# Kernel tuning notes

Hardware: AMD Instinct MI355X
Metric: run time of the kernel (lower is better)

## Reference

```python
import jax, jax.numpy as jnp
import numpy as np

N, n, D1, D2 = 16, 1024, 64, 64


def setup_inputs() -> dict:
    key = jax.random.key(0)
    ks = jax.random.split(key, 17)
    f = lambda k, shape: jax.random.normal(k, shape, dtype=jnp.float32)
    return {
        "A": f(ks[0], (N, n, n)),
        "X": f(ks[1], (N, n, D1)),
        "coeffs": f(ks[2], (5,)),
        "wA1": f(ks[3], (1, D1)),
        "wA2": f(ks[4], (1, D1)),
        "w11": f(ks[5], (D2, D1)),
        "w12": f(ks[6], (D2, D1)),
        "w13": f(ks[7], (D2, 1)),
        "w14": f(ks[8], (D2, 1)),
        "w15": f(ks[9], (D2, 1)),
        "w16": f(ks[10], (D2, 1)),
        "w21": f(ks[11], (D2, D1)),
        "w22": f(ks[12], (D2, D1)),
        "w23": f(ks[13], (D2, 1)),
        "w24": f(ks[14], (D2, 1)),
        "w25": f(ks[15], (D2, 1)),
        "w26": f(ks[16], (D2, 1)),
    }


def reference(A, X, coeffs, wA1, wA2, w11, w12, w13, w14, w15, w16,
              w21, w22, w23, w24, w25, w26):
    nn_ = A.shape[-1]
    diag = jnp.diagonal(A, axis1=-2, axis2=-1)          # (N, n)
    mean_diag = diag.mean(-1)                            # (N,)
    rowmean = A.mean(-1)                                 # (N, n) mean over columns
    mean_all = rowmean.mean(-1)                          # (N,)
    mean_X = X.mean(1)                                   # (N, D1)

    p1 = X @ wA1[0]                                      # (N, n)   Linear(D1->1) per node
    p2 = mean_X @ wA2[0]                                 # (N,)     Linear(D1->1) on mean

    # adjacency transform: scalar-weighted A + scalar stats + symmetrized row stats
    A_t = (coeffs[0] * A
           + (coeffs[1] * mean_all + coeffs[2] * mean_diag + p2)[:, None, None]
           + coeffs[3] * (rowmean[:, None, :] + rowmean[:, :, None])
           + coeffs[4] * (diag[:, None, :] + diag[:, :, None])
           + p1[:, None, :] + p1[:, :, None])             # (N, n, n)

    def node_transform(w_x, w_mx, w_col, w_diag, w_mdiag, w_mall):
        per_graph = (mean_X @ w_mx.T                      # (N, D2)
                     + mean_diag[:, None] * w_mdiag[:, 0][None, :]
                     + mean_all[:, None] * w_mall[:, 0][None, :])
        return (jnp.einsum('bnd,ed->bne', X, w_x)         # (N, n, D2)
                + rowmean[:, :, None] * w_col[:, 0]
                + diag[:, :, None] * w_diag[:, 0]
                + per_graph[:, None, :])

    X1_t = node_transform(w11, w12, w13, w14, w15, w16)
    X2_t = node_transform(w21, w22, w23, w24, w25, w26)

    out = A_t @ X2_t / nn_ + X1_t                         # (N, n, D2)
    return (A_t, out)
```

## Files before the change

kernel.cpp:

```cpp
#include <hip/hip_runtime.h>
#include <hip/hip_bf16.h>

#define NGRAPH 16
#define NNODE 1024
#define DDIM 64

typedef __attribute__((ext_vector_type(8))) short bf16x8;
typedef __attribute__((ext_vector_type(4))) float f32x4;

#define OFF_ROWSUM 0
#define OFF_DIAG   16384
#define OFF_P1     32768
#define OFF_R      49152
#define OFF_CS     65536
#define OFF_S      73728
#define OFF_PG1    73792
#define OFF_PG2    74816
#define OFF_S2P    75840
#define OFF_R2P    92224
#define OFF_S2N    108608
#define OFF_R2N    109632
#define OFF_BASE0  110656
#define OFF_X2T    1159232

__device__ __forceinline__ unsigned short f2bf(float f) {
    unsigned int u = __float_as_uint(f);
    u = (u + 0x7fffu + ((u >> 16) & 1u)) >> 16;
    return (unsigned short)u;
}

__device__ __forceinline__ float wave_reduce(float v) {
    #pragma unroll
    for (int off = 32; off; off >>= 1) v += __shfl_down(v, off, 64);
    return v;
}

__global__ __launch_bounds__(256) void k1_rowstats(const float* __restrict__ A,
                                                   float* __restrict__ rowsum,
                                                   float* __restrict__ diagv) {
    int row  = blockIdx.x * 4 + (threadIdx.x >> 6);
    int lane = threadIdx.x & 63;
    const float4* b4 = (const float4*)(A + (size_t)row * NNODE);
    float sum = 0.f;
    #pragma unroll
    for (int it = 0; it < 4; ++it) {
        float4 v = b4[lane + it * 64];
        sum += v.x + v.y + v.z + v.w;
    }
    sum = wave_reduce(sum);
    if (lane == 0) {
        rowsum[row] = sum;
        int i = row & (NNODE - 1);
        diagv[row] = ((const float*)b4)[i];
    }
}

__global__ __launch_bounds__(256) void k1b_xstats(const float* __restrict__ X,
                                                  const float* __restrict__ wA1,
                                                  float* __restrict__ p1,
                                                  float* __restrict__ colsum_part) {
    int b    = blockIdx.x >> 3;
    int blk  = blockIdx.x & 7;
    int wv   = threadIdx.x >> 6;
    int lane = threadIdx.x & 63;
    float w = wA1[lane];
    float cs = 0.f;
    int row0 = blk * 128 + wv * 32;
    const float* Xb = X + (size_t)b * NNODE * DDIM;
    for (int rI = 0; rI < 32; ++rI) {
        int i = row0 + rI;
        float x = Xb[i * DDIM + lane];
        cs += x;
        float v = wave_reduce(x * w);
        if (lane == 0) p1[b * NNODE + i] = v;
    }
    __shared__ float csl[4][64];
    csl[wv][lane] = cs;
    __syncthreads();
    if (threadIdx.x < 64) {
        float t = csl[0][lane] + csl[1][lane] + csl[2][lane] + csl[3][lane];
        colsum_part[(b * 8 + blk) * 64 + lane] = t;
    }
}

__global__ __launch_bounds__(64) void k2a_graph(const float* __restrict__ rowsum,
                                                const float* __restrict__ diagv,
                                                const float* __restrict__ colsum_part,
                                                const float* __restrict__ coeffs,
                                                const float* __restrict__ wA2,
                                                const float* __restrict__ w12,
                                                const float* __restrict__ w15,
                                                const float* __restrict__ w16,
                                                const float* __restrict__ w22,
                                                const float* __restrict__ w25,
                                                const float* __restrict__ w26,
                                                float* __restrict__ s_out,
                                                float* __restrict__ pg1,
                                                float* __restrict__ pg2) {
    int b = blockIdx.x;
    int lane = threadIdx.x;
    float sa = 0.f, sd = 0.f;
    for (int i = lane; i < NNODE; i += 64) {
        sa += rowsum[b * NNODE + i];
        sd += diagv[b * NNODE + i];
    }
    sa = wave_reduce(sa); sd = wave_reduce(sd);
    sa = __shfl(sa, 0, 64); sd = __shfl(sd, 0, 64);
    float mean_all  = sa * (1.f / ((float)NNODE * (float)NNODE));
    float mean_diag = sd * (1.f / (float)NNODE);

    float mx = 0.f;
    for (int k = 0; k < 8; ++k) mx += colsum_part[(b * 8 + k) * 64 + lane];
    mx *= (1.f / (float)NNODE);
    __shared__ float mxs[64];
    mxs[lane] = mx;
    __syncthreads();

    float p2v = wave_reduce(mx * wA2[lane]);
    p2v = __shfl(p2v, 0, 64);
    float s = coeffs[1] * mean_all + coeffs[2] * mean_diag + p2v;
    if (lane == 0) s_out[b] = s;

    float a1 = 0.f, a2 = 0.f;
    for (int d = 0; d < 64; ++d) {
        float m = mxs[d];
        a1 += m * w12[lane * 64 + d];
        a2 += m * w22[lane * 64 + d];
    }
    pg1[b * 64 + lane] = a1 + mean_diag * w15[lane] + mean_all * w16[lane];
    pg2[b * 64 + lane] = a2 + mean_diag * w25[lane] + mean_all * w26[lane];
}

__global__ __launch_bounds__(256) void k2b_nodes(const float* __restrict__ X,
                                                 const float* __restrict__ coeffs,
                                                 const float* __restrict__ w11,
                                                 const float* __restrict__ w21,
                                                 const float* __restrict__ w13,
                                                 const float* __restrict__ w14,
                                                 const float* __restrict__ w23,
                                                 const float* __restrict__ w24,
                                                 const float* __restrict__ pg1,
                                                 const float* __restrict__ pg2,
                                                 const float* __restrict__ rowsum,
                                                 const float* __restrict__ diagv,
                                                 const float* __restrict__ p1g,
                                                 float* __restrict__ rws,
                                                 float* __restrict__ base0,
                                                 unsigned short* __restrict__ x2tg,
                                                 float* __restrict__ S2part,
                                                 float* __restrict__ R2part) {
    __shared__ float Xl[64][68];
    __shared__ float w1l[64][68];
    __shared__ float w2l[64][68];
    __shared__ unsigned short X2Tl[64][68];
    __shared__ float rm_l[64], dg_l[64], r_l[64];
    __shared__ float redS[4][64], redR[4][64];

    int b    = blockIdx.x >> 4;
    int tile = blockIdx.x & 15;
    int i0   = tile * 64;
    int tid  = threadIdx.x;
    int e    = tid & 63;
    int wv   = tid >> 6;

    const float* Xg = X + (size_t)b * (NNODE * DDIM) + (size_t)i0 * DDIM;
    #pragma unroll
    for (int it = 0; it < 4; ++it) {
        int g   = it * 256 + tid;
        int row = g >> 4;
        int c4  = (g & 15) << 2;
        float4 v  = ((const float4*)Xg)[g];
        *(float4*)&Xl[row][c4] = v;
        float4 v1 = ((const float4*)w11)[g];
        *(float4*)&w1l[row][c4] = v1;
        float4 v2 = ((const float4*)w21)[g];
        *(float4*)&w2l[row][c4] = v2;
    }
    float c3 = coeffs[3], c4c = coeffs[4];
    if (tid < 64) {
        float rs  = rowsum[b * NNODE + i0 + tid];
        float dgv = diagv[b * NNODE + i0 + tid];
        float rmv = rs * (1.f / (float)NNODE);
        rm_l[tid] = rmv;
        dg_l[tid] = dgv;
        float rv = c3 * rmv + c4c * dgv + p1g[b * NNODE + i0 + tid];
        r_l[tid] = rv;
        rws[b * NNODE + i0 + tid] = rv;
    }
    float w13e = w13[e], w14e = w14[e], w23e = w23[e], w24e = w24[e];
    float pg1e = pg1[b * 64 + e], pg2e = pg2[b * 64 + e];
    __syncthreads();

    float acc1[16], acc2[16];
    #pragma unroll
    for (int t = 0; t < 16; ++t) { acc1[t] = 0.f; acc2[t] = 0.f; }

    for (int d0 = 0; d0 < 64; d0 += 4) {
        float4 w1v = *(const float4*)&w1l[e][d0];
        float4 w2v = *(const float4*)&w2l[e][d0];
        #pragma unroll
        for (int t = 0; t < 16; ++t) {
            int li = wv + 4 * t;
            float4 xv = *(const float4*)&Xl[li][d0];
            acc1[t] += xv.x * w1v.x + xv.y * w1v.y + xv.z * w1v.z + xv.w * w1v.w;
            acc2[t] += xv.x * w2v.x + xv.y * w2v.y + xv.z * w2v.z + xv.w * w2v.w;
        }
    }

    float s2acc = 0.f, r2acc = 0.f;
    #pragma unroll
    for (int t = 0; t < 16; ++t) {
        int li = wv + 4 * t;
        int i  = i0 + li;
        float rmv = rm_l[li], dgv = dg_l[li];
        float x2t = acc2[t] + rmv * w23e + dgv * w24e + pg2e;
        float b0  = acc1[t] + rmv * w13e + dgv * w14e + pg1e;
        base0[((size_t)(b * NNODE + i)) * 64 + e] = b0;
        X2Tl[e][li] = f2bf(x2t);
        s2acc += x2t;
        r2acc += r_l[li] * x2t;
    }
    redS[wv][e] = s2acc;
    redR[wv][e] = r2acc;
    __syncthreads();

    for (int k = 0; k < 16; ++k) {
        int ep = wv * 16 + k;
        unsigned short v = X2Tl[ep][e];
        x2tg[((size_t)(b * 64 + ep)) * NNODE + i0 + e] = v;
    }
    if (tid < 64) {
        float s2 = redS[0][tid] + redS[1][tid] + redS[2][tid] + redS[3][tid];
        float r2 = redR[0][tid] + redR[1][tid] + redR[2][tid] + redR[3][tid];
        S2part[(b * 16 + tile) * 64 + tid] = s2;
        R2part[(b * 16 + tile) * 64 + tid] = r2;
    }
}

__global__ __launch_bounds__(64) void k2c_reduce(const float* __restrict__ S2part,
                                                 const float* __restrict__ R2part,
                                                 float* __restrict__ S2n,
                                                 float* __restrict__ R2n) {
    int b = blockIdx.x, e = threadIdx.x;
    float s2 = 0.f, r2 = 0.f;
    for (int t = 0; t < 16; ++t) {
        s2 += S2part[(b * 16 + t) * 64 + e];
        r2 += R2part[(b * 16 + t) * 64 + e];
    }
    S2n[b * 64 + e] = s2 * (1.f / (float)NNODE);
    R2n[b * 64 + e] = r2 * (1.f / (float)NNODE);
}

__global__ __launch_bounds__(256) void k4_main(const float* __restrict__ A,
                                               const float* __restrict__ coeffs,
                                               const float* __restrict__ sArr,
                                               const float* __restrict__ rArr,
                                               const unsigned short* __restrict__ x2tg,
                                               const float* __restrict__ base0,
                                               const float* __restrict__ S2n,
                                               const float* __restrict__ R2n,
                                               float* __restrict__ At,
                                               float* __restrict__ outp) {
    __shared__ unsigned short Al[16][136];
    __shared__ unsigned short X2l[64][136];
    __shared__ float r_lds[1024];

    int b    = blockIdx.x >> 6;
    int tile = blockIdx.x & 63;
    int i0   = tile * 16;
    int tid  = threadIdx.x;

    float4 rv = ((const float4*)(rArr + b * NNODE))[tid];
    *(float4*)&r_lds[tid * 4] = rv;

    float sb  = sArr[b];
    float c0  = coeffs[0];
    float c0n = c0 * (1.f / (float)NNODE);

    int arow = tid >> 4;
    int acol = (tid & 15) * 8;
    const float* Ab  = A  + ((size_t)(b * NNODE + i0 + arow)) * NNODE + acol;
    float*       Atb = At + ((size_t)(b * NNODE + i0 + arow)) * NNODE + acol;
    int xe = tid >> 2;
    int xc = (tid & 3) * 32;
    const unsigned short* X2g = x2tg + ((size_t)(b * 64 + xe)) * NNODE + xc;

    int lane = tid & 63, wv = tid >> 6;
    int m = lane & 15, quad = lane >> 4;
    int e0 = wv << 4;

    f32x4 acc = {0.f, 0.f, 0.f, 0.f};

    for (int kt = 0; kt < 8; ++kt) {
        __syncthreads();

        float4 a0 = *(const float4*)(Ab + kt * 128);
        float4 a1 = *(const float4*)(Ab + kt * 128 + 4);
        float  ri = r_lds[i0 + arow];
        int cidx = kt * 128 + acol;
        float4 rj0 = *(const float4*)&r_lds[cidx];
        float4 rj1 = *(const float4*)&r_lds[cidx + 4];
        float bse = sb + ri;
        float4 t0, t1;
        t0.x = c0 * a0.x + bse + rj0.x; t0.y = c0 * a0.y + bse + rj0.y;
        t0.z = c0 * a0.z + bse + rj0.z; t0.w = c0 * a0.w + bse + rj0.w;
        t1.x = c0 * a1.x + bse + rj1.x; t1.y = c0 * a1.y + bse + rj1.y;
        t1.z = c0 * a1.z + bse + rj1.z; t1.w = c0 * a1.w + bse + rj1.w;
        *(float4*)(Atb + kt * 128)     = t0;
        *(float4*)(Atb + kt * 128 + 4) = t1;

        unsigned int p0 = (unsigned int)f2bf(a0.x) | ((unsigned int)f2bf(a0.y) << 16);
        unsigned int p1 = (unsigned int)f2bf(a0.z) | ((unsigned int)f2bf(a0.w) << 16);
        unsigned int p2 = (unsigned int)f2bf(a1.x) | ((unsigned int)f2bf(a1.y) << 16);
        unsigned int p3 = (unsigned int)f2bf(a1.z) | ((unsigned int)f2bf(a1.w) << 16);
        uint4 pk = {p0, p1, p2, p3};
        *(uint4*)&Al[arow][acol] = pk;

        #pragma unroll
        for (int q = 0; q < 4; ++q) {
            uint4 v = *(const uint4*)(X2g + (size_t)kt * 128 + q * 8);
            *(uint4*)&X2l[xe][xc + q * 8] = v;
        }
        __syncthreads();

        #pragma unroll
        for (int ks = 0; ks < 4; ++ks) {
            int k0 = ks * 32 + quad * 8;
            bf16x8 av = *(const bf16x8*)&Al[m][k0];
            bf16x8 bv = *(const bf16x8*)&X2l[e0 + m][k0];
            acc = __builtin_amdgcn_mfma_f32_16x16x32_bf16(av, bv, acc, 0, 0, 0);
        }
    }

    int e = e0 + m;
    float s2 = S2n[b * 64 + e];
    float r2 = R2n[b * 64 + e];
    #pragma unroll
    for (int reg = 0; reg < 4; ++reg) {
        int i = i0 + quad * 4 + reg;
        float v = acc[reg] * c0n
                + base0[((size_t)(b * NNODE + i)) * 64 + e]
                + (sb + r_lds[i]) * s2 + r2;
        outp[((size_t)(b * NNODE + i)) * 64 + e] = v;
    }
}

extern "C" void kernel_launch(void* const* d_in, const int* in_sizes, int n_in,
                              void* d_out, int out_size, void* d_ws, size_t ws_size,
                              hipStream_t stream) {
    const float* A      = (const float*)d_in[0];
    const float* X      = (const float*)d_in[1];
    const float* coeffs = (const float*)d_in[2];
    const float* wA1    = (const float*)d_in[3];
    const float* wA2    = (const float*)d_in[4];
    const float* w11    = (const float*)d_in[5];
    const float* w12    = (const float*)d_in[6];
    const float* w13    = (const float*)d_in[7];
    const float* w14    = (const float*)d_in[8];
    const float* w15    = (const float*)d_in[9];
    const float* w16    = (const float*)d_in[10];
    const float* w21    = (const float*)d_in[11];
    const float* w22    = (const float*)d_in[12];
    const float* w23    = (const float*)d_in[13];
    const float* w24    = (const float*)d_in[14];
    const float* w25    = (const float*)d_in[15];
    const float* w26    = (const float*)d_in[16];

    float* ws  = (float*)d_ws;
    float* At  = (float*)d_out;
    float* out = (float*)d_out + (size_t)NGRAPH * NNODE * NNODE;

    float* rowsum = ws + OFF_ROWSUM;
    float* diagv  = ws + OFF_DIAG;
    float* p1     = ws + OFF_P1;
    float* rws    = ws + OFF_R;
    float* cspart = ws + OFF_CS;
    float* sArr   = ws + OFF_S;
    float* pg1    = ws + OFF_PG1;
    float* pg2    = ws + OFF_PG2;
    float* S2part = ws + OFF_S2P;
    float* R2part = ws + OFF_R2P;
    float* S2n    = ws + OFF_S2N;
    float* R2n    = ws + OFF_R2N;
    float* base0  = ws + OFF_BASE0;
    unsigned short* x2tg = (unsigned short*)(ws + OFF_X2T);

    k1_rowstats<<<NGRAPH * NNODE / 4, 256, 0, stream>>>(A, rowsum, diagv);
    k1b_xstats<<<NGRAPH * 8, 256, 0, stream>>>(X, wA1, p1, cspart);
    k2a_graph<<<NGRAPH, 64, 0, stream>>>(rowsum, diagv, cspart, coeffs, wA2,
                                         w12, w15, w16, w22, w25, w26,
                                         sArr, pg1, pg2);
    k2b_nodes<<<NGRAPH * 16, 256, 0, stream>>>(X, coeffs, w11, w21, w13, w14, w23, w24,
                                               pg1, pg2, rowsum, diagv, p1,
                                               rws, base0, x2tg, S2part, R2part);
    k2c_reduce<<<NGRAPH, 64, 0, stream>>>(S2part, R2part, S2n, R2n);
    k4_main<<<NGRAPH * 64, 256, 0, stream>>>(A, coeffs, sArr, rws, x2tg, base0,
                                             S2n, R2n, At, out);
}
```

Measured before the change: 209.9 us.

## Fuse six launches into three, enlarge main tile, use nontemporal At stores

Merges the A row-stats and X-stats kernels into one launch. Per-graph statistics are recomputed redundantly inside each node-tile block, and the S2/R2 partial reduction moves into the main kernel, which removes three tiny launches and their serial dependencies. The main kernel now uses 512 threads with 32-row tiles, so each X2 tile loaded into LDS is shared by twice as many rows. The A_t output is written with nontemporal stores to reduce cache pollution. The cost is redundant per-graph work in every block and higher LDS and register pressure per block.

```diff
diff --git a/kernel.cpp b/kernel.cpp
--- a/kernel.cpp
+++ b/kernel.cpp
@@ -14,12 +14,8 @@
 #define OFF_R      49152
 #define OFF_CS     65536
 #define OFF_S      73728
-#define OFF_PG1    73792
-#define OFF_PG2    74816
 #define OFF_S2P    75840
 #define OFF_R2P    92224
-#define OFF_S2N    108608
-#define OFF_R2N    109632
 #define OFF_BASE0  110656
 #define OFF_X2T    1159232
 
@@ -35,126 +31,90 @@
     return v;
 }
 
-__global__ __launch_bounds__(256) void k1_rowstats(const float* __restrict__ A,
-                                                   float* __restrict__ rowsum,
-                                                   float* __restrict__ diagv) {
-    int row  = blockIdx.x * 4 + (threadIdx.x >> 6);
-    int lane = threadIdx.x & 63;
-    const float4* b4 = (const float4*)(A + (size_t)row * NNODE);
-    float sum = 0.f;
-    #pragma unroll
-    for (int it = 0; it < 4; ++it) {
-        float4 v = b4[lane + it * 64];
-        sum += v.x + v.y + v.z + v.w;
-    }
-    sum = wave_reduce(sum);
-    if (lane == 0) {
-        rowsum[row] = sum;
-        int i = row & (NNODE - 1);
-        diagv[row] = ((const float*)b4)[i];
-    }
-}
-
-__global__ __launch_bounds__(256) void k1b_xstats(const float* __restrict__ X,
-                                                  const float* __restrict__ wA1,
-                                                  float* __restrict__ p1,
-                                                  float* __restrict__ colsum_part) {
-    int b    = blockIdx.x >> 3;
-    int blk  = blockIdx.x & 7;
-    int wv   = threadIdx.x >> 6;
-    int lane = threadIdx.x & 63;
-    float w = wA1[lane];
-    float cs = 0.f;
-    int row0 = blk * 128 + wv * 32;
-    const float* Xb = X + (size_t)b * NNODE * DDIM;
-    for (int rI = 0; rI < 32; ++rI) {
-        int i = row0 + rI;
-        float x = Xb[i * DDIM + lane];
-        cs += x;
-        float v = wave_reduce(x * w);
-        if (lane == 0) p1[b * NNODE + i] = v;
-    }
-    __shared__ float csl[4][64];
-    csl[wv][lane] = cs;
-    __syncthreads();
-    if (threadIdx.x < 64) {
-        float t = csl[0][lane] + csl[1][lane] + csl[2][lane] + csl[3][lane];
-        colsum_part[(b * 8 + blk) * 64 + lane] = t;
-    }
-}
-
-__global__ __launch_bounds__(64) void k2a_graph(const float* __restrict__ rowsum,
+__global__ __launch_bounds__(256) void kA_stats(const float* __restrict__ A,
+                                                const float* __restrict__ X,
+                                                const float* __restrict__ wA1,
+                                                float* __restrict__ rowsum,
+                                                float* __restrict__ diagv,
+                                                float* __restrict__ p1,
+                                                float* __restrict__ colsum_part) {
+    if (blockIdx.x < NGRAPH * NNODE / 4) {
+        int row  = blockIdx.x * 4 + (threadIdx.x >> 6);
+        int lane = threadIdx.x & 63;
+        const float4* b4 = (const float4*)(A + (size_t)row * NNODE);
+        float sum = 0.f;
+        #pragma unroll
+        for (int it = 0; it < 4; ++it) {
+            float4 v = b4[lane + it * 64];
+            sum += v.x + v.y + v.z + v.w;
+        }
+        sum = wave_reduce(sum);
+        if (lane == 0) {
+            rowsum[row] = sum;
+            int i = row & (NNODE - 1);
+            diagv[row] = ((const float*)b4)[i];
+        }
+    } else {
+        int bid  = blockIdx.x - NGRAPH * NNODE / 4;
+        int b    = bid >> 3;
+        int blk  = bid & 7;
+        int wv   = threadIdx.x >> 6;
+        int lane = threadIdx.x & 63;
+        float w = wA1[lane];
+        float cs = 0.f;
+        int row0 = blk * 128 + wv * 32;
+        const float* Xb = X + (size_t)b * NNODE * DDIM;
+        for (int rI = 0; rI < 32; ++rI) {
+            int i = row0 + rI;
+            float x = Xb[i * DDIM + lane];
+            cs += x;
+            float v = wave_reduce(x * w);
+            if (lane == 0) p1[b * NNODE + i] = v;
+        }
+        __shared__ float csl[4][64];
+        csl[wv][lane] = cs;
+        __syncthreads();
+        if (threadIdx.x < 64) {
+            float t = csl[0][lane] + csl[1][lane] + csl[2][lane] + csl[3][lane];
+            colsum_part[(b * 8 + blk) * 64 + lane] = t;
+        }
+    }
+}
+
+__global__ __launch_bounds__(256) void kB_nodes(const float* __restrict__ X,
+                                                const float* __restrict__ coeffs,
+                                                const float* __restrict__ wA2,
+                                                const float* __restrict__ w11,
+                                                const float* __restrict__ w12,
+                                                const float* __restrict__ w13,
+                                                const float* __restrict__ w14,
+                                                const float* __restrict__ w15,
+                                                const float* __restrict__ w16,
+                                                const float* __restrict__ w21,
+                                                const float* __restrict__ w22,
+                                                const float* __restrict__ w23,
+                                                const float* __restrict__ w24,
+                                                const float* __restrict__ w25,
+                                                const float* __restrict__ w26,
+                                                const float* __restrict__ rowsum,
                                                 const float* __restrict__ diagv,
                                                 const float* __restrict__ colsum_part,
-                                                const float* __restrict__ coeffs,
-                                                const float* __restrict__ wA2,
-                                                const float* __restrict__ w12,
-                                                const float* __restrict__ w15,
-                                                const float* __restrict__ w16,
-                                                const float* __restrict__ w22,
-                                                const float* __restrict__ w25,
-                                                const float* __restrict__ w26,
-                                                float* __restrict__ s_out,
-                                                float* __restrict__ pg1,
-                                                float* __restrict__ pg2) {
-    int b = blockIdx.x;
-    int lane = threadIdx.x;
-    float sa = 0.f, sd = 0.f;
-    for (int i = lane; i < NNODE; i += 64) {
-        sa += rowsum[b * NNODE + i];
-        sd += diagv[b * NNODE + i];
-    }
-    sa = wave_reduce(sa); sd = wave_reduce(sd);
-    sa = __shfl(sa, 0, 64); sd = __shfl(sd, 0, 64);
-    float mean_all  = sa * (1.f / ((float)NNODE * (float)NNODE));
-    float mean_diag = sd * (1.f / (float)NNODE);
-
-    float mx = 0.f;
-    for (int k = 0; k < 8; ++k) mx += colsum_part[(b * 8 + k) * 64 + lane];
-    mx *= (1.f / (float)NNODE);
-    __shared__ float mxs[64];
-    mxs[lane] = mx;
-    __syncthreads();
-
-    float p2v = wave_reduce(mx * wA2[lane]);
-    p2v = __shfl(p2v, 0, 64);
-    float s = coeffs[1] * mean_all + coeffs[2] * mean_diag + p2v;
-    if (lane == 0) s_out[b] = s;
-
-    float a1 = 0.f, a2 = 0.f;
-    for (int d = 0; d < 64; ++d) {
-        float m = mxs[d];
-        a1 += m * w12[lane * 64 + d];
-        a2 += m * w22[lane * 64 + d];
-    }
-    pg1[b * 64 + lane] = a1 + mean_diag * w15[lane] + mean_all * w16[lane];
-    pg2[b * 64 + lane] = a2 + mean_diag * w25[lane] + mean_all * w26[lane];
-}
-
-__global__ __launch_bounds__(256) void k2b_nodes(const float* __restrict__ X,
-                                                 const float* __restrict__ coeffs,
-                                                 const float* __restrict__ w11,
-                                                 const float* __restrict__ w21,
-                                                 const float* __restrict__ w13,
-                                                 const float* __restrict__ w14,
-                                                 const float* __restrict__ w23,
-                                                 const float* __restrict__ w24,
-                                                 const float* __restrict__ pg1,
-                                                 const float* __restrict__ pg2,
-                                                 const float* __restrict__ rowsum,
-                                                 const float* __restrict__ diagv,
-                                                 const float* __restrict__ p1g,
-                                                 float* __restrict__ rws,
-                                                 float* __restrict__ base0,
-                                                 unsigned short* __restrict__ x2tg,
-                                                 float* __restrict__ S2part,
-                                                 float* __restrict__ R2part) {
+                                                const float* __restrict__ p1g,
+                                                float* __restrict__ rws,
+                                                float* __restrict__ base0,
+                                                unsigned short* __restrict__ x2tg,
+                                                float* __restrict__ S2part,
+                                                float* __restrict__ R2part,
+                                                float* __restrict__ sArr) {
     __shared__ float Xl[64][68];
     __shared__ float w1l[64][68];
     __shared__ float w2l[64][68];
     __shared__ unsigned short X2Tl[64][68];
     __shared__ float rm_l[64], dg_l[64], r_l[64];
     __shared__ float redS[4][64], redR[4][64];
+    __shared__ float redA[4], redD[4];
+    __shared__ float mxs[64], p2s;
+    __shared__ float pg1_l[64], pg2_l[64];
 
     int b    = blockIdx.x >> 4;
     int tile = blockIdx.x & 15;
@@ -176,6 +136,36 @@
         float4 v2 = ((const float4*)w21)[g];
         *(float4*)&w2l[row][c4] = v2;
     }
+
+    float sa = 0.f, sd = 0.f;
+    for (int i = tid; i < NNODE; i += 256) {
+        sa += rowsum[b * NNODE + i];
+        sd += diagv[b * NNODE + i];
+    }
+    sa = wave_reduce(sa); sd = wave_reduce(sd);
+    if (e == 0) { redA[wv] = sa; redD[wv] = sd; }
+    if (tid < 64) {
+        float mx = 0.f;
+        for (int k = 0; k < 8; ++k) mx += colsum_part[(b * 8 + k) * 64 + tid];
+        mxs[tid] = mx * (1.f / (float)NNODE);
+    }
+    __syncthreads();
+    float mean_all  = (redA[0] + redA[1] + redA[2] + redA[3]) * (1.f / ((float)NNODE * (float)NNODE));
+    float mean_diag = (redD[0] + redD[1] + redD[2] + redD[3]) * (1.f / (float)NNODE);
+    if (tid < 64) {
+        float v = wave_reduce(mxs[tid] * wA2[tid]);
+        if (tid == 0) p2s = v;
+    }
+    if (tid < 64) {
+        float a1 = 0.f, a2 = 0.f;
+        for (int d = 0; d < 64; ++d) {
+            float m = mxs[d];
+            a1 += m * w12[tid * 64 + d];
+            a2 += m * w22[tid * 64 + d];
+        }
+        pg1_l[tid] = a1 + mean_diag * w15[tid] + mean_all * w16[tid];
+        pg2_l[tid] = a2 + mean_diag * w25[tid] + mean_all * w26[tid];
+    }
     float c3 = coeffs[3], c4c = coeffs[4];
     if (tid < 64) {
         float rs  = rowsum[b * NNODE + i0 + tid];
@@ -187,9 +177,12 @@
         r_l[tid] = rv;
         rws[b * NNODE + i0 + tid] = rv;
     }
+    __syncthreads();
+    if (tile == 0 && tid == 0)
+        sArr[b] = coeffs[1] * mean_all + coeffs[2] * mean_diag + p2s;
+
     float w13e = w13[e], w14e = w14[e], w23e = w23[e], w24e = w24[e];
-    float pg1e = pg1[b * 64 + e], pg2e = pg2[b * 64 + e];
-    __syncthreads();
+    float pg1e = pg1_l[e], pg2e = pg2_l[e];
 
     float acc1[16], acc2[16];
     #pragma unroll
@@ -237,41 +230,40 @@
     }
 }
 
-__global__ __launch_bounds__(64) void k2c_reduce(const float* __restrict__ S2part,
-                                                 const float* __restrict__ R2part,
-                                                 float* __restrict__ S2n,
-                                                 float* __restrict__ R2n) {
-    int b = blockIdx.x, e = threadIdx.x;
-    float s2 = 0.f, r2 = 0.f;
-    for (int t = 0; t < 16; ++t) {
-        s2 += S2part[(b * 16 + t) * 64 + e];
-        r2 += R2part[(b * 16 + t) * 64 + e];
-    }
-    S2n[b * 64 + e] = s2 * (1.f / (float)NNODE);
-    R2n[b * 64 + e] = r2 * (1.f / (float)NNODE);
-}
-
-__global__ __launch_bounds__(256) void k4_main(const float* __restrict__ A,
+__global__ __launch_bounds__(512) void kC_main(const float* __restrict__ A,
                                                const float* __restrict__ coeffs,
                                                const float* __restrict__ sArr,
                                                const float* __restrict__ rArr,
                                                const unsigned short* __restrict__ x2tg,
                                                const float* __restrict__ base0,
-                                               const float* __restrict__ S2n,
-                                               const float* __restrict__ R2n,
+                                               const float* __restrict__ S2part,
+                                               const float* __restrict__ R2part,
                                                float* __restrict__ At,
                                                float* __restrict__ outp) {
-    __shared__ unsigned short Al[16][136];
+    __shared__ unsigned short Al[32][136];
     __shared__ unsigned short X2l[64][136];
     __shared__ float r_lds[1024];
-
-    int b    = blockIdx.x >> 6;
-    int tile = blockIdx.x & 63;
-    int i0   = tile * 16;
+    __shared__ float s2_lds[64], r2_lds[64];
+
+    int b    = blockIdx.x >> 5;
+    int tile = blockIdx.x & 31;
+    int i0   = tile * 32;
     int tid  = threadIdx.x;
 
-    float4 rv = ((const float4*)(rArr + b * NNODE))[tid];
-    *(float4*)&r_lds[tid * 4] = rv;
+    if (tid < 256) {
+        float4 rv = ((const float4*)(rArr + b * NNODE))[tid];
+        *(float4*)&r_lds[tid * 4] = rv;
+    } else if (tid < 320) {
+        int e = tid - 256;
+        float s2 = 0.f, r2 = 0.f;
+        #pragma unroll
+        for (int t = 0; t < 16; ++t) {
+            s2 += S2part[(b * 16 + t) * 64 + e];
+            r2 += R2part[(b * 16 + t) * 64 + e];
+        }
+        s2_lds[e] = s2 * (1.f / (float)NNODE);
+        r2_lds[e] = r2 * (1.f / (float)NNODE);
+    }
 
     float sb  = sArr[b];
     float c0  = coeffs[0];
@@ -281,13 +273,14 @@
     int acol = (tid & 15) * 8;
     const float* Ab  = A  + ((size_t)(b * NNODE + i0 + arow)) * NNODE + acol;
     float*       Atb = At + ((size_t)(b * NNODE + i0 + arow)) * NNODE + acol;
-    int xe = tid >> 2;
-    int xc = (tid & 3) * 32;
+    int xe = tid >> 3;
+    int xc = (tid & 7) * 16;
     const unsigned short* X2g = x2tg + ((size_t)(b * 64 + xe)) * NNODE + xc;
 
     int lane = tid & 63, wv = tid >> 6;
     int m = lane & 15, quad = lane >> 4;
-    int e0 = wv << 4;
+    int rh = wv >> 2;
+    int e0 = (wv & 3) * 16;
 
     f32x4 acc = {0.f, 0.f, 0.f, 0.f};
 
@@ -301,13 +294,13 @@
         float4 rj0 = *(const float4*)&r_lds[cidx];
         float4 rj1 = *(const float4*)&r_lds[cidx + 4];
         float bse = sb + ri;
-        float4 t0, t1;
+        f32x4 t0, t1;
         t0.x = c0 * a0.x + bse + rj0.x; t0.y = c0 * a0.y + bse + rj0.y;
         t0.z = c0 * a0.z + bse + rj0.z; t0.w = c0 * a0.w + bse + rj0.w;
         t1.x = c0 * a1.x + bse + rj1.x; t1.y = c0 * a1.y + bse + rj1.y;
         t1.z = c0 * a1.z + bse + rj1.z; t1.w = c0 * a1.w + bse + rj1.w;
-        *(float4*)(Atb + kt * 128)     = t0;
-        *(float4*)(Atb + kt * 128 + 4) = t1;
+        __builtin_nontemporal_store(t0, (f32x4*)(Atb + kt * 128));
+        __builtin_nontemporal_store(t1, (f32x4*)(Atb + kt * 128 + 4));
 
         unsigned int p0 = (unsigned int)f2bf(a0.x) | ((unsigned int)f2bf(a0.y) << 16);
         unsigned int p1 = (unsigned int)f2bf(a0.z) | ((unsigned int)f2bf(a0.w) << 16);
@@ -316,28 +309,27 @@
         uint4 pk = {p0, p1, p2, p3};
         *(uint4*)&Al[arow][acol] = pk;
 
-        #pragma unroll
-        for (int q = 0; q < 4; ++q) {
-            uint4 v = *(const uint4*)(X2g + (size_t)kt * 128 + q * 8);
-            *(uint4*)&X2l[xe][xc + q * 8] = v;
-        }
+        uint4 xv0 = *(const uint4*)(X2g + (size_t)kt * 128);
+        uint4 xv1 = *(const uint4*)(X2g + (size_t)kt * 128 + 8);
+        *(uint4*)&X2l[xe][xc]     = xv0;
+        *(uint4*)&X2l[xe][xc + 8] = xv1;
         __syncthreads();
 
         #pragma unroll
         for (int ks = 0; ks < 4; ++ks) {
             int k0 = ks * 32 + quad * 8;
-            bf16x8 av = *(const bf16x8*)&Al[m][k0];
+            bf16x8 av = *(const bf16x8*)&Al[rh * 16 + m][k0];
             bf16x8 bv = *(const bf16x8*)&X2l[e0 + m][k0];
             acc = __builtin_amdgcn_mfma_f32_16x16x32_bf16(av, bv, acc, 0, 0, 0);
         }
     }
 
     int e = e0 + m;
-    float s2 = S2n[b * 64 + e];
-    float r2 = R2n[b * 64 + e];
+    float s2 = s2_lds[e];
+    float r2 = r2_lds[e];
     #pragma unroll
     for (int reg = 0; reg < 4; ++reg) {
-        int i = i0 + quad * 4 + reg;
+        int i = i0 + rh * 16 + quad * 4 + reg;
         float v = acc[reg] * c0n
                 + base0[((size_t)(b * NNODE + i)) * 64 + e]
                 + (sb + r_lds[i]) * s2 + r2;
@@ -376,24 +368,18 @@
     float* rws    = ws + OFF_R;
     float* cspart = ws + OFF_CS;
     float* sArr   = ws + OFF_S;
-    float* pg1    = ws + OFF_PG1;
-    float* pg2    = ws + OFF_PG2;
     float* S2part = ws + OFF_S2P;
     float* R2part = ws + OFF_R2P;
-    float* S2n    = ws + OFF_S2N;
-    float* R2n    = ws + OFF_R2N;
     float* base0  = ws + OFF_BASE0;
     unsigned short* x2tg = (unsigned short*)(ws + OFF_X2T);
 
-    k1_rowstats<<<NGRAPH * NNODE / 4, 256, 0, stream>>>(A, rowsum, diagv);
-    k1b_xstats<<<NGRAPH * 8, 256, 0, stream>>>(X, wA1, p1, cspart);
-    k2a_graph<<<NGRAPH, 64, 0, stream>>>(rowsum, diagv, cspart, coeffs, wA2,
-                                         w12, w15, w16, w22, w25, w26,
-                                         sArr, pg1, pg2);
-    k2b_nodes<<<NGRAPH * 16, 256, 0, stream>>>(X, coeffs, w11, w21, w13, w14, w23, w24,
-                                               pg1, pg2, rowsum, diagv, p1,
-                                               rws, base0, x2tg, S2part, R2part);
-    k2c_reduce<<<NGRAPH, 64, 0, stream>>>(S2part, R2part, S2n, R2n);
-    k4_main<<<NGRAPH * 64, 256, 0, stream>>>(A, coeffs, sArr, rws, x2tg, base0,
-                                             S2n, R2n, At, out);
-}
+    kA_stats<<<NGRAPH * NNODE / 4 + NGRAPH * 8, 256, 0, stream>>>(
+        A, X, wA1, rowsum, diagv, p1, cspart);
+    kB_nodes<<<NGRAPH * 16, 256, 0, stream>>>(
+        X, coeffs, wA2, w11, w12, w13, w14, w15, w16,
+        w21, w22, w23, w24, w25, w26,
+        rowsum, diagv, cspart, p1,
+        rws, base0, x2tg, S2part, R2part, sArr);
+    kC_main<<<NGRAPH * 32, 512, 0, stream>>>(
+        A, coeffs, sArr, rws, x2tg, base0, S2part, R2part, At, out);
+}
```

Result: slower. 217.8 us (+3.8%).
